# Kernel optimization log

Measured on AMD Instinct MI355X. Metric: run time of the kernel, lower is better.

The kernel has to match this reference:

```python
import jax, jax.numpy as jnp
import numpy as np

N = 50000      # nodes
E = 600000     # edges
D_IN = 128
D_H = 128
D_OUT = 64
HEADS = 2
NEG_SLOPE = 0.2  # PyG GATConv default leaky_relu slope
BN_EPS = 1e-5


def setup_inputs() -> dict:
    key = jax.random.key(0)
    ks = jax.random.split(key, 24)
    w = lambda i, shape: (jax.random.normal(ks[i], shape, jnp.float32) * 0.1)
    return {
        "x": jax.random.normal(ks[0], (N, D_IN), jnp.float32),
        "edge_index": jax.random.randint(ks[1], (2, E), 0, N, jnp.int64),
        "W_gcn1": w(2, (D_IN, D_H)),
        "b_gcn1": jnp.zeros((D_H,), jnp.float32),
        "bn1_gamma": jax.random.uniform(ks[3], (D_H,), jnp.float32, 0.5, 1.5),
        "bn1_beta": w(4, (D_H,)),
        "bn1_mean": w(5, (D_H,)),
        "bn1_var": jax.random.uniform(ks[6], (D_H,), jnp.float32, 0.5, 1.5),
        "W_gat1": w(7, (D_H, HEADS * D_H)),
        "a_src1": w(8, (HEADS, D_H)),
        "a_dst1": w(9, (HEADS, D_H)),
        "b_gat1": jnp.zeros((D_H,), jnp.float32),
        "W_gcn2": w(10, (D_H, D_H)),
        "b_gcn2": jnp.zeros((D_H,), jnp.float32),
        "bn2_gamma": jax.random.uniform(ks[11], (D_H,), jnp.float32, 0.5, 1.5),
        "bn2_beta": w(12, (D_H,)),
        "bn2_mean": w(13, (D_H,)),
        "bn2_var": jax.random.uniform(ks[14], (D_H,), jnp.float32, 0.5, 1.5),
        "W_gat2": w(15, (D_H, HEADS * D_OUT)),
        "a_src2": w(16, (HEADS, D_OUT)),
        "a_dst2": w(17, (HEADS, D_OUT)),
        "b_gat2": jnp.zeros((D_OUT,), jnp.float32),
    }


def _add_self_loops(edge_index):
    loop = jnp.arange(N, dtype=edge_index.dtype)
    src = jnp.concatenate([edge_index[0], loop])
    dst = jnp.concatenate([edge_index[1], loop])
    return src, dst


def _gcn(x, edge_index, W, b):
    # PyG GCNConv: add self-loops, symmetric D^-1/2 (A+I) D^-1/2 normalization
    src, dst = _add_self_loops(edge_index)
    deg = jax.ops.segment_sum(jnp.ones_like(dst, x.dtype), dst, num_segments=N)
    dinv = jax.lax.rsqrt(jnp.maximum(deg, 1.0))  # deg >= 1 with self-loops
    norm = dinv[src] * dinv[dst]                 # [E+N]
    h = x @ W                                    # [N, C]
    out = jax.ops.segment_sum(h[src] * norm[:, None], dst, num_segments=N)
    return out + b


def _gat(x, edge_index, W, a_src, a_dst, b, out_ch):
    # PyG GATConv (concat=False): per-head attention, segment softmax over dst,
    # mean across heads. Dropout off (eval mode).
    h = (x @ W).reshape(N, HEADS, out_ch)                 # [N, H, C]
    al_s = jnp.einsum('nhc,hc->nh', h, a_src)             # [N, H]
    al_d = jnp.einsum('nhc,hc->nh', h, a_dst)             # [N, H]
    src, dst = _add_self_loops(edge_index)
    e = al_s[src] + al_d[dst]                             # [E+N, H]
    e = jnp.where(e > 0, e, NEG_SLOPE * e)                # leaky_relu
    m = jax.ops.segment_max(e, dst, num_segments=N)       # [N, H]
    ex = jnp.exp(e - m[dst])
    denom = jax.ops.segment_sum(ex, dst, num_segments=N)  # [N, H]
    alpha = ex / denom[dst]                               # [E+N, H]
    out = jax.ops.segment_sum(h[src] * alpha[:, :, None], dst, num_segments=N)
    return out.mean(axis=1) + b                           # concat=False -> mean


def _bn_eval(x, gamma, beta, mean, var):
    return (x - mean) * jax.lax.rsqrt(var + BN_EPS) * gamma + beta


def reference(x, edge_index, W_gcn1, b_gcn1, bn1_gamma, bn1_beta, bn1_mean, bn1_var,
              W_gat1, a_src1, a_dst1, b_gat1, W_gcn2, b_gcn2,
              bn2_gamma, bn2_beta, bn2_mean, bn2_var,
              W_gat2, a_src2, a_dst2, b_gat2):
    h = _gcn(x, edge_index, W_gcn1, b_gcn1)
    h = jax.nn.relu(_bn_eval(h, bn1_gamma, bn1_beta, bn1_mean, bn1_var))
    h = jax.nn.relu(_gat(h, edge_index, W_gat1, a_src1, a_dst1, b_gat1, D_H))
    h = _gcn(h, edge_index, W_gcn2, b_gcn2)
    h = jax.nn.relu(_bn_eval(h, bn2_gamma, bn2_beta, bn2_mean, bn2_var))
    h = _gat(h, edge_index, W_gat2, a_src2, a_dst2, b_gat2, D_OUT)
    return jax.nn.log_softmax(h, axis=1)
```

## Files before the change

kernel.cpp:

```cpp
#include <hip/hip_runtime.h>
#include <hip/hip_bf16.h>

#define N_NODES 50000
#define N_EDGES 600000

typedef short bf16x8 __attribute__((ext_vector_type(8)));
typedef float f32x4 __attribute__((ext_vector_type(4)));

__device__ __forceinline__ float leaky(float e) { return fmaxf(e, 0.2f * e); }
__device__ __forceinline__ unsigned short f2b(float f) {
  __hip_bfloat16 h = __float2bfloat16(f);
  return *reinterpret_cast<unsigned short*>(&h);
}
__device__ __forceinline__ float blo(unsigned int u) { return __uint_as_float(u << 16); }
__device__ __forceinline__ float bhi(unsigned int u) { return __uint_as_float(u & 0xffff0000u); }

__global__ void k_convert(const int* __restrict__ e, int* __restrict__ src32,
                          int* __restrict__ dst32, int* __restrict__ deg,
                          const float* __restrict__ W1, const float* __restrict__ WG1,
                          const float* __restrict__ W2, const float* __restrict__ WG2,
                          unsigned short* __restrict__ Wt1, unsigned short* __restrict__ WtG1,
                          unsigned short* __restrict__ Wt2, unsigned short* __restrict__ WtG2,
                          const float* b1, const float* g1, const float* be1, const float* m1,
                          const float* v1, const float* b2, const float* g2, const float* be2,
                          const float* m2, const float* v2, float* sc1, float* sh1,
                          float* sc2, float* sh2,
                          const float* as1, const float* ad1, const float* as2,
                          const float* ad2, float* was1, float* wad1, float* was2,
                          float* wad2) {
  __shared__ int sflag;
  int tid = threadIdx.x;
  if (tid < 64) {
    int idx = 1 + 2 * tid * 4096;
    int v = e[idx];
    unsigned long long nz = __ballot(v != 0);
    if (tid == 0) sflag = (nz == 0ULL) ? 1 : 0;
  }
  __syncthreads();
  int f = sflag;
  int i = blockIdx.x * 256 + tid;
  if (i < N_EDGES) {
    int s, d;
    if (f) { s = e[2 * i]; d = e[2 * (N_EDGES + i)]; }
    else   { s = e[i];     d = e[N_EDGES + i]; }
    src32[i] = s;
    dst32[i] = d;
    atomicAdd(&deg[d], 1);
  }
  if (i < 16384) {
    int k = i >> 7, c = i & 127;
    Wt1[c * 128 + k] = f2b(W1[i]);
  } else if (i < 49152) {
    int l = i - 16384;
    int k = l >> 8, c8 = l & 255;
    int head = c8 >> 7, cc = c8 & 127;
    WtG1[cc * 256 + head * 128 + k] = f2b(WG1[l]);
  } else if (i < 65536) {
    int l = i - 49152;
    int k = l >> 7, c = l & 127;
    Wt2[c * 128 + k] = f2b(W2[l]);
  } else if (i < 81920) {
    int l = i - 65536;
    int k = l >> 7, c = l & 127;
    WtG2[c * 128 + k] = f2b(WG2[l]);
  } else if (i < 82048) {
    int c = i - 81920;
    float s = g1[c] * rsqrtf(v1[c] + 1e-5f);
    sc1[c] = s;
    sh1[c] = (b1[c] - m1[c]) * s + be1[c];
  } else if (i < 82176) {
    int c = i - 82048;
    float s = g2[c] * rsqrtf(v2[c] + 1e-5f);
    sc2[c] = s;
    sh2[c] = (b2[c] - m2[c]) * s + be2[c];
  } else if (i < 82688) {
    int j = i - 82176;
    int k = j & 127;
    int vec = j >> 7;
    const float* Wr = (vec < 2) ? (WG1 + k * 256) : (WG2 + k * 128);
    const float* av = (vec == 0) ? as1 : (vec == 1) ? ad1 : (vec == 2) ? as2 : ad2;
    float* op = (vec == 0) ? was1 : (vec == 1) ? wad1 : (vec == 2) ? was2 : wad2;
    int hl = (vec < 2) ? 128 : 64;
    float s0 = 0.f, s1 = 0.f;
    for (int c = 0; c < hl; c += 4) {
      float4 wv = *(const float4*)(Wr + c);
      float4 a4 = *(const float4*)(av + c);
      s0 += wv.x * a4.x + wv.y * a4.y + wv.z * a4.z + wv.w * a4.w;
    }
    for (int c = 0; c < hl; c += 4) {
      float4 wv = *(const float4*)(Wr + hl + c);
      float4 a4 = *(const float4*)(av + hl + c);
      s1 += wv.x * a4.x + wv.y * a4.y + wv.z * a4.z + wv.w * a4.w;
    }
    op[2 * k] = s0;
    op[2 * k + 1] = s1;
  }
}

__global__ void k_offsets(const int* __restrict__ deg, int* __restrict__ gbase,
                          int* __restrict__ roff, int* __restrict__ cursor,
                          float* __restrict__ dinv) {
  __shared__ int s[256];
  __shared__ int base;
  int t = threadIdx.x;
  int i = blockIdx.x * 256 + t;
  int v = (i < N_NODES) ? deg[i] : 0;
  s[t] = v;
  __syncthreads();
  for (int o = 1; o < 256; o <<= 1) {
    int x = (t >= o) ? s[t - o] : 0;
    __syncthreads();
    s[t] += x;
    __syncthreads();
  }
  if (t == 255) base = atomicAdd(gbase, s[255]);
  __syncthreads();
  int off = base + s[t] - v;
  if (i < N_NODES) {
    roff[i] = off;
    cursor[i] = off;
    dinv[i] = rsqrtf((float)v + 1.f);
  }
}
__global__ void k_fill(const int* __restrict__ src, const int* __restrict__ dst,
                       int* __restrict__ cursor, int2* __restrict__ aen,
                       const float* __restrict__ dinv) {
  int e = blockIdx.x * 256 + threadIdx.x;
  if (e < N_EDGES) {
    int s = src[e], d = dst[e];
    int pos = atomicAdd(&cursor[d], 1);
    aen[pos] = make_int2(s, __float_as_int(dinv[s]));
  }
}

__device__ __forceinline__ float4 ld4(const float* X, size_t idx) {
  return *(const float4*)(X + idx);
}
__device__ __forceinline__ float4 ld4(const unsigned short* X, size_t idx) {
  uint2 r = *(const uint2*)(X + idx);
  return make_float4(blo(r.x), bhi(r.x), blo(r.y), bhi(r.y));
}

template <typename TX>
__global__ __launch_bounds__(256, 4) void gemm_mfma(const TX* __restrict__ X,
                                                    const unsigned short* __restrict__ Wt,
                                                    unsigned short* __restrict__ Hb) {
  __shared__ __align__(16) short smem[64 * 136];
  int tid = threadIdx.x;
  int row0 = blockIdx.x * 64;
  for (int i = tid; i < 2048; i += 256) {
    int r = i >> 5;
    int k4 = (i & 31) * 4;
    int row = row0 + r;
    float4 v = make_float4(0.f, 0.f, 0.f, 0.f);
    if (row < N_NODES) v = ld4(X, (size_t)row * 128 + k4);
    uint2 p;
    p.x = (unsigned int)f2b(v.x) | ((unsigned int)f2b(v.y) << 16);
    p.y = (unsigned int)f2b(v.z) | ((unsigned int)f2b(v.w) << 16);
    *(uint2*)&smem[r * 136 + k4] = p;
  }
  int wave = tid >> 6, lane = tid & 63;
  int m = lane & 15, quad = lane >> 4;
  int c0 = wave * 32;
  bf16x8 b[2][4];
#pragma unroll
  for (int ct = 0; ct < 2; ++ct) {
    const unsigned short* wp = Wt + (size_t)(c0 + ct * 16 + m) * 128 + quad * 8;
#pragma unroll
    for (int kk = 0; kk < 4; ++kk) b[ct][kk] = *(const bf16x8*)(wp + kk * 32);
  }
  __syncthreads();
#pragma unroll
  for (int rt = 0; rt < 4; ++rt) {
    bf16x8 a[4];
#pragma unroll
    for (int kk = 0; kk < 4; ++kk)
      a[kk] = *(const bf16x8*)&smem[(rt * 16 + m) * 136 + kk * 32 + quad * 8];
    f32x4 acc[2];
#pragma unroll
    for (int ct = 0; ct < 2; ++ct) acc[ct] = (f32x4){0.f, 0.f, 0.f, 0.f};
#pragma unroll
    for (int ct = 0; ct < 2; ++ct)
#pragma unroll
      for (int kk = 0; kk < 4; ++kk)
        acc[ct] = __builtin_amdgcn_mfma_f32_16x16x32_bf16(a[kk], b[ct][kk], acc[ct], 0, 0, 0);
    int rbase = row0 + rt * 16 + quad * 4;
#pragma unroll
    for (int ct = 0; ct < 2; ++ct) {
#pragma unroll
      for (int reg = 0; reg < 4; ++reg) {
        int row = rbase + reg;
        if (row < N_NODES)
          Hb[(size_t)row * 128 + c0 + ct * 16 + m] = f2b(acc[ct][reg]);
      }
    }
  }
}

__global__ __launch_bounds__(256, 4) void gemm_k256(const unsigned short* __restrict__ Q,
                                                    const unsigned short* __restrict__ Wt,
                                                    const float* __restrict__ bias,
                                                    unsigned short* __restrict__ G) {
  __shared__ __align__(16) short smem[64 * 136];
  int tid = threadIdx.x;
  int row0 = blockIdx.x * 64;
  int wave = tid >> 6, lane = tid & 63;
  int m = lane & 15, quad = lane >> 4;
  int c0 = wave * 32;
  f32x4 acc[4][2];
#pragma unroll
  for (int rt = 0; rt < 4; ++rt)
#pragma unroll
    for (int ct = 0; ct < 2; ++ct) acc[rt][ct] = (f32x4){0.f, 0.f, 0.f, 0.f};
#pragma unroll
  for (int half = 0; half < 2; ++half) {
    if (half) __syncthreads();
    for (int i = tid; i < 2048; i += 256) {
      int r = i >> 5;
      int k4 = (i & 31) * 4;
      int row = row0 + r;
      uint2 p = make_uint2(0u, 0u);
      if (row < N_NODES) p = *(const uint2*)(Q + (size_t)row * 256 + half * 128 + k4);
      *(uint2*)&smem[r * 136 + k4] = p;
    }
    bf16x8 b[2][4];
#pragma unroll
    for (int ct = 0; ct < 2; ++ct) {
      const unsigned short* wp =
          Wt + (size_t)(c0 + ct * 16 + m) * 256 + half * 128 + quad * 8;
#pragma unroll
      for (int kk = 0; kk < 4; ++kk) b[ct][kk] = *(const bf16x8*)(wp + kk * 32);
    }
    __syncthreads();
#pragma unroll
    for (int rt = 0; rt < 4; ++rt) {
      bf16x8 a[4];
#pragma unroll
      for (int kk = 0; kk < 4; ++kk)
        a[kk] = *(const bf16x8*)&smem[(rt * 16 + m) * 136 + kk * 32 + quad * 8];
#pragma unroll
      for (int ct = 0; ct < 2; ++ct)
#pragma unroll
        for (int kk = 0; kk < 4; ++kk)
          acc[rt][ct] =
              __builtin_amdgcn_mfma_f32_16x16x32_bf16(a[kk], b[ct][kk], acc[rt][ct], 0, 0, 0);
    }
  }
#pragma unroll
  for (int rt = 0; rt < 4; ++rt) {
    int rbase = row0 + rt * 16 + quad * 4;
#pragma unroll
    for (int ct = 0; ct < 2; ++ct) {
      int col = c0 + ct * 16 + m;
      float bs = bias[col];
#pragma unroll
      for (int reg = 0; reg < 4; ++reg) {
        int row = rbase + reg;
        if (row < N_NODES)
          G[(size_t)row * 128 + col] = f2b(fmaxf(acc[rt][ct][reg] + bs, 0.f));
      }
    }
  }
}

__global__ __launch_bounds__(256) void gcn_pull(const unsigned short* __restrict__ Hb,
                                                const int2* __restrict__ aen,
                                                const int* __restrict__ roff,
                                                const int* __restrict__ deg,
                                                const float* __restrict__ dinv,
                                                const float* __restrict__ sc,
                                                const float* __restrict__ sh,
                                                const float* __restrict__ was,
                                                const float* __restrict__ wad,
                                                float* __restrict__ als,
                                                float* __restrict__ ald,
                                                unsigned short* __restrict__ out) {
  int wv = (blockIdx.x * 256 + threadIdx.x) >> 6;
  int lane = threadIdx.x & 63;
  int q4 = lane >> 4, l16 = lane & 15;
  int qb = lane & 48, l7 = lane & 7;
  int i = 4 * wv + q4;
  if (i >= N_NODES) return;
  int off = roff[i], end = off + deg[i];
  float di = dinv[i];
  uint4 u = *(const uint4*)((const char*)Hb + (unsigned)i * 256u + l16 * 16u);
  float a0 = blo(u.x) * di, a1 = bhi(u.x) * di;
  float a2 = blo(u.y) * di, a3 = bhi(u.y) * di;
  float a4 = blo(u.z) * di, a5 = bhi(u.z) * di;
  float a6 = blo(u.w) * di, a7 = bhi(u.w) * di;
  int j = off;
  int nfull = (end - off) >> 3;
  int2 ae = make_int2(i, 0);
  if (l7 < end - j) ae = aen[j + l7];
  for (int t = 0; t < nfull; ++t) {
    int ss[8];
#pragma unroll
    for (int k = 0; k < 8; ++k) ss[k] = __shfl(ae.x, qb + k, 64);
    float ww[8];
#pragma unroll
    for (int k = 0; k < 8; ++k) ww[k] = __shfl(__int_as_float(ae.y), qb + k, 64);
    uint4 vv[8];
#pragma unroll
    for (int k = 0; k < 8; ++k)
      vv[k] = *(const uint4*)((const char*)Hb + (unsigned)ss[k] * 256u + l16 * 16u);
    j += 8;
    if (l7 < end - j) ae = aen[j + l7];
#pragma unroll
    for (int k = 0; k < 8; ++k) {
      a0 = fmaf(blo(vv[k].x), ww[k], a0); a1 = fmaf(bhi(vv[k].x), ww[k], a1);
      a2 = fmaf(blo(vv[k].y), ww[k], a2); a3 = fmaf(bhi(vv[k].y), ww[k], a3);
      a4 = fmaf(blo(vv[k].z), ww[k], a4); a5 = fmaf(bhi(vv[k].z), ww[k], a5);
      a6 = fmaf(blo(vv[k].w), ww[k], a6); a7 = fmaf(bhi(vv[k].w), ww[k], a7);
    }
  }
  int rem = end - j;
  if (rem) {
    int ss[8];
#pragma unroll
    for (int k = 0; k < 8; ++k) ss[k] = __shfl(ae.x, qb + k, 64);
    float ww[8];
#pragma unroll
    for (int k = 0; k < 8; ++k) ww[k] = __shfl(__int_as_float(ae.y), qb + k, 64);
    uint4 vv[8];
#pragma unroll
    for (int k = 0; k < 8; ++k)
      if (k < rem)
        vv[k] = *(const uint4*)((const char*)Hb + (unsigned)ss[k] * 256u + l16 * 16u);
#pragma unroll
    for (int k = 0; k < 8; ++k)
      if (k < rem) {
        a0 = fmaf(blo(vv[k].x), ww[k], a0); a1 = fmaf(bhi(vv[k].x), ww[k], a1);
        a2 = fmaf(blo(vv[k].y), ww[k], a2); a3 = fmaf(bhi(vv[k].y), ww[k], a3);
        a4 = fmaf(blo(vv[k].z), ww[k], a4); a5 = fmaf(bhi(vv[k].z), ww[k], a5);
        a6 = fmaf(blo(vv[k].w), ww[k], a6); a7 = fmaf(bhi(vv[k].w), ww[k], a7);
      }
  }
  int c0 = l16 * 8;
  float4 sca = *(const float4*)(sc + c0), scb = *(const float4*)(sc + c0 + 4);
  float4 sha = *(const float4*)(sh + c0), shb = *(const float4*)(sh + c0 + 4);
  float t0 = fmaxf(fmaf(a0 * di, sca.x, sha.x), 0.f);
  float t1 = fmaxf(fmaf(a1 * di, sca.y, sha.y), 0.f);
  float t2 = fmaxf(fmaf(a2 * di, sca.z, sha.z), 0.f);
  float t3 = fmaxf(fmaf(a3 * di, sca.w, sha.w), 0.f);
  float t4 = fmaxf(fmaf(a4 * di, scb.x, shb.x), 0.f);
  float t5 = fmaxf(fmaf(a5 * di, scb.y, shb.y), 0.f);
  float t6 = fmaxf(fmaf(a6 * di, scb.z, shb.z), 0.f);
  float t7 = fmaxf(fmaf(a7 * di, scb.w, shb.w), 0.f);
  float4 w0 = *(const float4*)(was + 2 * c0);
  float4 w1 = *(const float4*)(was + 2 * c0 + 4);
  float4 w2 = *(const float4*)(was + 2 * c0 + 8);
  float4 w3 = *(const float4*)(was + 2 * c0 + 12);
  float sl0 = t0 * w0.x + t1 * w0.z + t2 * w1.x + t3 * w1.z +
              t4 * w2.x + t5 * w2.z + t6 * w3.x + t7 * w3.z;
  float sl1 = t0 * w0.y + t1 * w0.w + t2 * w1.y + t3 * w1.w +
              t4 * w2.y + t5 * w2.w + t6 * w3.y + t7 * w3.w;
  w0 = *(const float4*)(wad + 2 * c0);
  w1 = *(const float4*)(wad + 2 * c0 + 4);
  w2 = *(const float4*)(wad + 2 * c0 + 8);
  w3 = *(const float4*)(wad + 2 * c0 + 12);
  float dl0 = t0 * w0.x + t1 * w0.z + t2 * w1.x + t3 * w1.z +
              t4 * w2.x + t5 * w2.z + t6 * w3.x + t7 * w3.z;
  float dl1 = t0 * w0.y + t1 * w0.w + t2 * w1.y + t3 * w1.w +
              t4 * w2.y + t5 * w2.w + t6 * w3.y + t7 * w3.w;
#pragma unroll
  for (int mask = 1; mask <= 8; mask <<= 1) {
    sl0 += __shfl_xor(sl0, mask, 64);
    sl1 += __shfl_xor(sl1, mask, 64);
    dl0 += __shfl_xor(dl0, mask, 64);
    dl1 += __shfl_xor(dl1, mask, 64);
  }
  if (l16 == 0) {
    *(float2*)(als + 2 * i) = make_float2(sl0, sl1);
    *(float2*)(ald + 2 * i) = make_float2(dl0, dl1);
  }
  uint4 pw;
  pw.x = (unsigned int)f2b(t0) | ((unsigned int)f2b(t1) << 16);
  pw.y = (unsigned int)f2b(t2) | ((unsigned int)f2b(t3) << 16);
  pw.z = (unsigned int)f2b(t4) | ((unsigned int)f2b(t5) << 16);
  pw.w = (unsigned int)f2b(t6) | ((unsigned int)f2b(t7) << 16);
  *(uint4*)(out + (size_t)i * 128 + l16 * 8) = pw;
}

__global__ __launch_bounds__(256) void gat1_pull(const unsigned short* __restrict__ P,
                                                 const int2* __restrict__ aen,
                                                 const int* __restrict__ roff,
                                                 const int* __restrict__ deg,
                                                 const float* __restrict__ als,
                                                 const float* __restrict__ ald,
                                                 unsigned short* __restrict__ Q) {
  int wv = (blockIdx.x * 256 + threadIdx.x) >> 6;
  int lane = threadIdx.x & 63;
  int q4 = lane >> 4, l16 = lane & 15;
  int qb = lane & 48, l7 = lane & 7;
  int i = 4 * wv + q4;
  if (i >= N_NODES) return;
  int off = roff[i], end = off + deg[i];
  float2 dif = *(const float2*)(ald + 2 * i);
  float p0 = 0.f, p1 = 0.f;
  float g0 = 0.f, g1 = 0.f, g2 = 0.f, g3 = 0.f,
        g4 = 0.f, g5 = 0.f, g6 = 0.f, g7 = 0.f;
  float h0 = 0.f, h1 = 0.f, h2 = 0.f, h3 = 0.f,
        h4 = 0.f, h5 = 0.f, h6 = 0.f, h7 = 0.f;
  int j = off;
  int nfull = (end - off) >> 3;
  int2 ae = make_int2(i, 0);
  float2 av = make_float2(-1e30f, -1e30f);
  if (l7 < end - j) {
    ae = aen[j + l7];
    av = *(const float2*)(als + 2 * ae.x);
  }
  for (int t = 0; t < nfull; ++t) {
    int ss[8];
#pragma unroll
    for (int k = 0; k < 8; ++k) ss[k] = __shfl(ae.x, qb + k, 64);
    uint4 vv[8];
#pragma unroll
    for (int k = 0; k < 8; ++k)
      vv[k] = *(const uint4*)((const char*)P + (unsigned)ss[k] * 256u + l16 * 16u);
    float q0 = __expf(leaky(av.x + dif.x));
    float q1 = __expf(leaky(av.y + dif.y));
    j += 8;
    if (l7 < end - j) {
      ae = aen[j + l7];
      av = *(const float2*)(als + 2 * ae.x);
    }
#pragma unroll
    for (int k = 0; k < 8; ++k) {
      float b0 = __shfl(q0, qb + k, 64);
      float b1 = __shfl(q1, qb + k, 64);
      p0 += b0; p1 += b1;
      float c0 = blo(vv[k].x), c1 = bhi(vv[k].x);
      float c2 = blo(vv[k].y), c3 = bhi(vv[k].y);
      float c4 = blo(vv[k].z), c5 = bhi(vv[k].z);
      float c6 = blo(vv[k].w), c7 = bhi(vv[k].w);
      g0 = fmaf(b0, c0, g0); h0 = fmaf(b1, c0, h0);
      g1 = fmaf(b0, c1, g1); h1 = fmaf(b1, c1, h1);
      g2 = fmaf(b0, c2, g2); h2 = fmaf(b1, c2, h2);
      g3 = fmaf(b0, c3, g3); h3 = fmaf(b1, c3, h3);
      g4 = fmaf(b0, c4, g4); h4 = fmaf(b1, c4, h4);
      g5 = fmaf(b0, c5, g5); h5 = fmaf(b1, c5, h5);
      g6 = fmaf(b0, c6, g6); h6 = fmaf(b1, c6, h6);
      g7 = fmaf(b0, c7, g7); h7 = fmaf(b1, c7, h7);
    }
  }
  int rem = end - j;
  if (rem) {
    int ss[8];
#pragma unroll
    for (int k = 0; k < 8; ++k) ss[k] = __shfl(ae.x, qb + k, 64);
    uint4 vv[8];
#pragma unroll
    for (int k = 0; k < 8; ++k)
      if (k < rem)
        vv[k] = *(const uint4*)((const char*)P + (unsigned)ss[k] * 256u + l16 * 16u);
    float q0 = __expf(leaky(av.x + dif.x));
    float q1 = __expf(leaky(av.y + dif.y));
#pragma unroll
    for (int k = 0; k < 8; ++k)
      if (k < rem) {
        float b0 = __shfl(q0, qb + k, 64);
        float b1 = __shfl(q1, qb + k, 64);
        p0 += b0; p1 += b1;
        float c0 = blo(vv[k].x), c1 = bhi(vv[k].x);
        float c2 = blo(vv[k].y), c3 = bhi(vv[k].y);
        float c4 = blo(vv[k].z), c5 = bhi(vv[k].z);
        float c6 = blo(vv[k].w), c7 = bhi(vv[k].w);
        g0 = fmaf(b0, c0, g0); h0 = fmaf(b1, c0, h0);
        g1 = fmaf(b0, c1, g1); h1 = fmaf(b1, c1, h1);
        g2 = fmaf(b0, c2, g2); h2 = fmaf(b1, c2, h2);
        g3 = fmaf(b0, c3, g3); h3 = fmaf(b1, c3, h3);
        g4 = fmaf(b0, c4, g4); h4 = fmaf(b1, c4, h4);
        g5 = fmaf(b0, c5, g5); h5 = fmaf(b1, c5, h5);
        g6 = fmaf(b0, c6, g6); h6 = fmaf(b1, c6, h6);
        g7 = fmaf(b0, c7, g7); h7 = fmaf(b1, c7, h7);
      }
  }
  float2 ai = *(const float2*)(als + 2 * i);
  float es0 = __expf(leaky(ai.x + dif.x));
  float es1 = __expf(leaky(ai.y + dif.y));
  float r0 = 0.5f / (p0 + es0);
  float r1 = 0.5f / (p1 + es1);
  uint4 u = *(const uint4*)((const char*)P + (unsigned)i * 256u + l16 * 16u);
  float c0 = blo(u.x), c1 = bhi(u.x), c2 = blo(u.y), c3 = bhi(u.y);
  float c4 = blo(u.z), c5 = bhi(u.z), c6 = blo(u.w), c7 = bhi(u.w);
  g0 = (g0 + es0 * c0) * r0; g1 = (g1 + es0 * c1) * r0;
  g2 = (g2 + es0 * c2) * r0; g3 = (g3 + es0 * c3) * r0;
  g4 = (g4 + es0 * c4) * r0; g5 = (g5 + es0 * c5) * r0;
  g6 = (g6 + es0 * c6) * r0; g7 = (g7 + es0 * c7) * r0;
  h0 = (h0 + es1 * c0) * r1; h1 = (h1 + es1 * c1) * r1;
  h2 = (h2 + es1 * c2) * r1; h3 = (h3 + es1 * c3) * r1;
  h4 = (h4 + es1 * c4) * r1; h5 = (h5 + es1 * c5) * r1;
  h6 = (h6 + es1 * c6) * r1; h7 = (h7 + es1 * c7) * r1;
  uint4 pw;
  pw.x = (unsigned int)f2b(g0) | ((unsigned int)f2b(g1) << 16);
  pw.y = (unsigned int)f2b(g2) | ((unsigned int)f2b(g3) << 16);
  pw.z = (unsigned int)f2b(g4) | ((unsigned int)f2b(g5) << 16);
  pw.w = (unsigned int)f2b(g6) | ((unsigned int)f2b(g7) << 16);
  *(uint4*)(Q + (size_t)i * 256 + l16 * 8) = pw;
  pw.x = (unsigned int)f2b(h0) | ((unsigned int)f2b(h1) << 16);
  pw.y = (unsigned int)f2b(h2) | ((unsigned int)f2b(h3) << 16);
  pw.z = (unsigned int)f2b(h4) | ((unsigned int)f2b(h5) << 16);
  pw.w = (unsigned int)f2b(h6) | ((unsigned int)f2b(h7) << 16);
  *(uint4*)(Q + (size_t)i * 256 + 128 + l16 * 8) = pw;
}

__global__ __launch_bounds__(256) void gat_pull64_lsm(const unsigned short* __restrict__ Hb,
                                                      const int2* __restrict__ aen,
                                                      const int* __restrict__ roff,
                                                      const int* __restrict__ deg,
                                                      const float* __restrict__ als,
                                                      const float* __restrict__ ald,
                                                      const float* __restrict__ bias,
                                                      float* __restrict__ out) {
  int wv = (blockIdx.x * 256 + threadIdx.x) >> 6;
  int lane = threadIdx.x & 63;
  int q4 = lane >> 4, l16 = lane & 15;
  int qb = lane & 48, l7 = lane & 7;
  int hh = l16 >> 3, p8 = l16 & 7;
  int i = 4 * wv + q4;
  if (i >= N_NODES) return;
  int off = roff[i], end = off + deg[i];
  unsigned cb2 = (unsigned)(hh * 64 + 8 * p8) * 2u;
  float2 dd = *(const float2*)(ald + 2 * i);
  float p = 0.f;
  float acc0 = 0.f, acc1 = 0.f, acc2 = 0.f, acc3 = 0.f;
  float acc4 = 0.f, acc5 = 0.f, acc6 = 0.f, acc7 = 0.f;
  int j = off;
  int nfull = (end - off) >> 3;
  int2 ae = make_int2(i, 0);
  float2 av = make_float2(-1e30f, -1e30f);
  if (l7 < end - j) {
    ae = aen[j + l7];
    av = *(const float2*)(als + 2 * ae.x);
  }
  for (int t = 0; t < nfull; ++t) {
    int ss[8];
#pragma unroll
    for (int k = 0; k < 8; ++k) ss[k] = __shfl(ae.x, qb + k, 64);
    uint4 vv[8];
#pragma unroll
    for (int k = 0; k < 8; ++k)
      vv[k] = *(const uint4*)((const char*)Hb + (unsigned)ss[k] * 256u + cb2);
    float q0 = __expf(leaky(av.x + dd.x));
    float q1 = __expf(leaky(av.y + dd.y));
    j += 8;
    if (l7 < end - j) {
      ae = aen[j + l7];
      av = *(const float2*)(als + 2 * ae.x);
    }
#pragma unroll
    for (int k = 0; k < 8; ++k) {
      float b0 = __shfl(q0, qb + k, 64);
      float b1 = __shfl(q1, qb + k, 64);
      float q = hh ? b1 : b0;
      p += q;
      acc0 = fmaf(q, blo(vv[k].x), acc0); acc1 = fmaf(q, bhi(vv[k].x), acc1);
      acc2 = fmaf(q, blo(vv[k].y), acc2); acc3 = fmaf(q, bhi(vv[k].y), acc3);
      acc4 = fmaf(q, blo(vv[k].z), acc4); acc5 = fmaf(q, bhi(vv[k].z), acc5);
      acc6 = fmaf(q, blo(vv[k].w), acc6); acc7 = fmaf(q, bhi(vv[k].w), acc7);
    }
  }
  int rem = end - j;
  if (rem) {
    int ss[8];
#pragma unroll
    for (int k = 0; k < 8; ++k) ss[k] = __shfl(ae.x, qb + k, 64);
    uint4 vv[8];
#pragma unroll
    for (int k = 0; k < 8; ++k)
      if (k < rem)
        vv[k] = *(const uint4*)((const char*)Hb + (unsigned)ss[k] * 256u + cb2);
    float q0 = __expf(leaky(av.x + dd.x));
    float q1 = __expf(leaky(av.y + dd.y));
#pragma unroll
    for (int k = 0; k < 8; ++k)
      if (k < rem) {
        float b0 = __shfl(q0, qb + k, 64);
        float b1 = __shfl(q1, qb + k, 64);
        float q = hh ? b1 : b0;
        p += q;
        acc0 = fmaf(q, blo(vv[k].x), acc0); acc1 = fmaf(q, bhi(vv[k].x), acc1);
        acc2 = fmaf(q, blo(vv[k].y), acc2); acc3 = fmaf(q, bhi(vv[k].y), acc3);
        acc4 = fmaf(q, blo(vv[k].z), acc4); acc5 = fmaf(q, bhi(vv[k].z), acc5);
        acc6 = fmaf(q, blo(vv[k].w), acc6); acc7 = fmaf(q, bhi(vv[k].w), acc7);
      }
  }
  float2 ai = *(const float2*)(als + 2 * i);
  float axs = hh ? ai.y : ai.x;
  float dh = hh ? dd.y : dd.x;
  float es = __expf(leaky(axs + dh));
  float rsel = 0.5f / (p + es);
  uint4 u = *(const uint4*)((const char*)Hb + (unsigned)i * 256u + cb2);
  acc0 = (acc0 + es * blo(u.x)) * rsel; acc1 = (acc1 + es * bhi(u.x)) * rsel;
  acc2 = (acc2 + es * blo(u.y)) * rsel; acc3 = (acc3 + es * bhi(u.y)) * rsel;
  acc4 = (acc4 + es * blo(u.z)) * rsel; acc5 = (acc5 + es * bhi(u.z)) * rsel;
  acc6 = (acc6 + es * blo(u.w)) * rsel; acc7 = (acc7 + es * bhi(u.w)) * rsel;
  acc0 += __shfl_xor(acc0, 8, 64); acc1 += __shfl_xor(acc1, 8, 64);
  acc2 += __shfl_xor(acc2, 8, 64); acc3 += __shfl_xor(acc3, 8, 64);
  acc4 += __shfl_xor(acc4, 8, 64); acc5 += __shfl_xor(acc5, 8, 64);
  acc6 += __shfl_xor(acc6, 8, 64); acc7 += __shfl_xor(acc7, 8, 64);
  float4 b0 = *(const float4*)(bias + 8 * p8);
  float4 b1 = *(const float4*)(bias + 8 * p8 + 4);
  float v0 = acc0 + b0.x, v1 = acc1 + b0.y, v2 = acc2 + b0.z, v3 = acc3 + b0.w;
  float v4 = acc4 + b1.x, v5 = acc5 + b1.y, v6 = acc6 + b1.z, v7 = acc7 + b1.w;
  float mv = fmaxf(fmaxf(fmaxf(v0, v1), fmaxf(v2, v3)),
                   fmaxf(fmaxf(v4, v5), fmaxf(v6, v7)));
#pragma unroll
  for (int mm = 4; mm > 0; mm >>= 1) mv = fmaxf(mv, __shfl_xor(mv, mm, 64));
  float sv = __expf(v0 - mv) + __expf(v1 - mv) + __expf(v2 - mv) + __expf(v3 - mv) +
             __expf(v4 - mv) + __expf(v5 - mv) + __expf(v6 - mv) + __expf(v7 - mv);
#pragma unroll
  for (int mm = 4; mm > 0; mm >>= 1) sv += __shfl_xor(sv, mm, 64);
  float ls = mv + __logf(sv);
  if (hh == 0) {
    *(float4*)(out + (size_t)i * 64 + 8 * p8) =
        make_float4(v0 - ls, v1 - ls, v2 - ls, v3 - ls);
    *(float4*)(out + (size_t)i * 64 + 8 * p8 + 4) =
        make_float4(v4 - ls, v5 - ls, v6 - ls, v7 - ls);
  }
}

extern "C" void kernel_launch(void* const* d_in, const int* in_sizes, int n_in, void* d_out,
                              int out_size, void* d_ws, size_t ws_size, hipStream_t stream) {
  const float* x      = (const float*)d_in[0];
  const int* eidx     = (const int*)d_in[1];
  const float* W_gcn1 = (const float*)d_in[2];
  const float* b_gcn1 = (const float*)d_in[3];
  const float* bn1_g  = (const float*)d_in[4];
  const float* bn1_b  = (const float*)d_in[5];
  const float* bn1_m  = (const float*)d_in[6];
  const float* bn1_v  = (const float*)d_in[7];
  const float* W_gat1 = (const float*)d_in[8];
  const float* a_src1 = (const float*)d_in[9];
  const float* a_dst1 = (const float*)d_in[10];
  const float* b_gat1 = (const float*)d_in[11];
  const float* W_gcn2 = (const float*)d_in[12];
  const float* b_gcn2 = (const float*)d_in[13];
  const float* bn2_g  = (const float*)d_in[14];
  const float* bn2_b  = (const float*)d_in[15];
  const float* bn2_m  = (const float*)d_in[16];
  const float* bn2_v  = (const float*)d_in[17];
  const float* W_gat2 = (const float*)d_in[18];
  const float* a_src2 = (const float*)d_in[19];
  const float* a_dst2 = (const float*)d_in[20];
  const float* b_gat2 = (const float*)d_in[21];

  char* ws = (char*)d_ws;
  size_t o = 0;
  auto take = [&](size_t bytes) {
    char* p = ws + o;
    o = (o + bytes + 255) & ~(size_t)255;
    return p;
  };
  int* srcs    = (int*)take((size_t)N_EDGES * 4);
  int* dstsb   = (int*)take((size_t)N_EDGES * 4);
  int* deg     = (int*)take((size_t)(N_NODES + 64) * 4);
  int* gbase   = deg + N_NODES;
  int* roff    = (int*)take((size_t)N_NODES * 4);
  int* cursor  = (int*)take((size_t)N_NODES * 4);
  int2* aen    = (int2*)take((size_t)N_EDGES * 8);
  float* dinv  = (float*)take((size_t)N_NODES * 4);
  float* als   = (float*)take((size_t)2 * N_NODES * 4);
  float* ald   = (float*)take((size_t)2 * N_NODES * 4);
  float* sc1   = (float*)take(128 * 4);
  float* sh1   = (float*)take(128 * 4);
  float* sc2   = (float*)take(128 * 4);
  float* sh2   = (float*)take(128 * 4);
  float* was1  = (float*)take(256 * 4);
  float* wad1  = (float*)take(256 * 4);
  float* was2  = (float*)take(256 * 4);
  float* wad2  = (float*)take(256 * 4);
  unsigned short* Wt1  = (unsigned short*)take((size_t)128 * 128 * 2);
  unsigned short* WtG1 = (unsigned short*)take((size_t)128 * 256 * 2);
  unsigned short* Wt2  = (unsigned short*)take((size_t)128 * 128 * 2);
  unsigned short* WtG2 = (unsigned short*)take((size_t)128 * 128 * 2);
  unsigned short* Hb   = (unsigned short*)take((size_t)N_NODES * 128 * 2);
  unsigned short* Pb   = (unsigned short*)take((size_t)N_NODES * 128 * 2);
  unsigned short* Qb   = (unsigned short*)take((size_t)N_NODES * 256 * 2);
  unsigned short* Gb   = (unsigned short*)take((size_t)N_NODES * 128 * 2);
  (void)ws_size; (void)in_sizes; (void)n_in; (void)out_size;

  int eb = (N_EDGES + 255) / 256;
  int nb = (N_NODES + 255) / 256;
  int qb = ((N_NODES + 3) / 4 + 3) / 4;
  int gb = (N_NODES + 63) / 64;

  hipMemsetAsync(deg, 0, (size_t)(N_NODES + 1) * 4, stream);
  k_convert<<<eb, 256, 0, stream>>>(eidx, srcs, dstsb, deg, W_gcn1, W_gat1, W_gcn2, W_gat2,
                                    Wt1, WtG1, Wt2, WtG2, b_gcn1, bn1_g, bn1_b, bn1_m, bn1_v,
                                    b_gcn2, bn2_g, bn2_b, bn2_m, bn2_v, sc1, sh1, sc2, sh2,
                                    a_src1, a_dst1, a_src2, a_dst2, was1, wad1, was2, wad2);
  k_offsets<<<nb, 256, 0, stream>>>(deg, gbase, roff, cursor, dinv);
  k_fill<<<eb, 256, 0, stream>>>(srcs, dstsb, cursor, aen, dinv);

  gemm_mfma<<<gb, 256, 0, stream>>>(x, Wt1, Hb);
  gcn_pull<<<qb, 256, 0, stream>>>(Hb, aen, roff, deg, dinv, sc1, sh1, was1, wad1,
                                   als, ald, Pb);
  gat1_pull<<<qb, 256, 0, stream>>>(Pb, aen, roff, deg, als, ald, Qb);
  gemm_k256<<<gb, 256, 0, stream>>>(Qb, WtG1, b_gat1, Gb);
  gemm_mfma<<<gb, 256, 0, stream>>>(Gb, Wt2, Hb);
  gcn_pull<<<qb, 256, 0, stream>>>(Hb, aen, roff, deg, dinv, sc2, sh2, was2, wad2,
                                   als, ald, Pb);
  gemm_mfma<<<gb, 256, 0, stream>>>(Pb, WtG2, Qb);
  gat_pull64_lsm<<<qb, 256, 0, stream>>>(Qb, aen, roff, deg, als, ald, b_gat2,
                                         (float*)d_out);
}
```

Baseline: 340.8 us.

## Reorder GCN2 as aggregate-then-transform and fuse GCN2/GAT2 GEMMs with LDS-staged stores

Layer-2 GCN now aggregates the GAT1 output first (A·G), then a single kernel applies W_gcn2, BN+ReLU, the W_gat2 GEMM and the attention logits, keeping the intermediate in LDS. This removes one GEMM launch and a full bf16 round trip of the intermediate. GEMM epilogues now stage results through shared memory so rows are written with coalesced 16-byte stores. Edge-index conversion no longer writes src/dst int32 copies; k_fill reads the original index array directly using a stored layout flag. The reordering changes where bf16 rounding happens, which slightly alters numerics.

```diff
diff --git a/kernel.cpp b/kernel.cpp
--- a/kernel.cpp
+++ b/kernel.cpp
@@ -15,8 +15,8 @@
 __device__ __forceinline__ float blo(unsigned int u) { return __uint_as_float(u << 16); }
 __device__ __forceinline__ float bhi(unsigned int u) { return __uint_as_float(u & 0xffff0000u); }
 
-__global__ void k_convert(const int* __restrict__ e, int* __restrict__ src32,
-                          int* __restrict__ dst32, int* __restrict__ deg,
+__global__ void k_convert(const int* __restrict__ e, int* __restrict__ deg,
+                          int* __restrict__ flag,
                           const float* __restrict__ W1, const float* __restrict__ WG1,
                           const float* __restrict__ W2, const float* __restrict__ WG2,
                           unsigned short* __restrict__ Wt1, unsigned short* __restrict__ WtG1,
@@ -39,12 +39,9 @@
   __syncthreads();
   int f = sflag;
   int i = blockIdx.x * 256 + tid;
+  if (i == 0) flag[0] = f;
   if (i < N_EDGES) {
-    int s, d;
-    if (f) { s = e[2 * i]; d = e[2 * (N_EDGES + i)]; }
-    else   { s = e[i];     d = e[N_EDGES + i]; }
-    src32[i] = s;
-    dst32[i] = d;
+    int d = f ? e[2 * (N_EDGES + i)] : e[N_EDGES + i];
     atomicAdd(&deg[d], 1);
   }
   if (i < 16384) {
@@ -122,27 +119,21 @@
     dinv[i] = rsqrtf((float)v + 1.f);
   }
 }
-__global__ void k_fill(const int* __restrict__ src, const int* __restrict__ dst,
+__global__ void k_fill(const int* __restrict__ e, const int* __restrict__ flag,
                        int* __restrict__ cursor, int2* __restrict__ aen,
                        const float* __restrict__ dinv) {
-  int e = blockIdx.x * 256 + threadIdx.x;
-  if (e < N_EDGES) {
-    int s = src[e], d = dst[e];
+  int f = flag[0];
+  int i = blockIdx.x * 256 + threadIdx.x;
+  if (i < N_EDGES) {
+    int s, d;
+    if (f) { s = e[2 * i]; d = e[2 * (N_EDGES + i)]; }
+    else   { s = e[i];     d = e[N_EDGES + i]; }
     int pos = atomicAdd(&cursor[d], 1);
     aen[pos] = make_int2(s, __float_as_int(dinv[s]));
   }
 }
 
-__device__ __forceinline__ float4 ld4(const float* X, size_t idx) {
-  return *(const float4*)(X + idx);
-}
-__device__ __forceinline__ float4 ld4(const unsigned short* X, size_t idx) {
-  uint2 r = *(const uint2*)(X + idx);
-  return make_float4(blo(r.x), bhi(r.x), blo(r.y), bhi(r.y));
-}
-
-template <typename TX>
-__global__ __launch_bounds__(256, 4) void gemm_mfma(const TX* __restrict__ X,
+__global__ __launch_bounds__(256, 4) void gemm_mfma(const float* __restrict__ X,
                                                     const unsigned short* __restrict__ Wt,
                                                     unsigned short* __restrict__ Hb) {
   __shared__ __align__(16) short smem[64 * 136];
@@ -153,7 +144,7 @@
     int k4 = (i & 31) * 4;
     int row = row0 + r;
     float4 v = make_float4(0.f, 0.f, 0.f, 0.f);
-    if (row < N_NODES) v = ld4(X, (size_t)row * 128 + k4);
+    if (row < N_NODES) v = *(const float4*)(X + (size_t)row * 128 + k4);
     uint2 p;
     p.x = (unsigned int)f2b(v.x) | ((unsigned int)f2b(v.y) << 16);
     p.y = (unsigned int)f2b(v.z) | ((unsigned int)f2b(v.w) << 16);
@@ -170,30 +161,37 @@
     for (int kk = 0; kk < 4; ++kk) b[ct][kk] = *(const bf16x8*)(wp + kk * 32);
   }
   __syncthreads();
+  f32x4 acc[4][2];
+#pragma unroll
+  for (int rt = 0; rt < 4; ++rt)
+#pragma unroll
+    for (int ct = 0; ct < 2; ++ct) acc[rt][ct] = (f32x4){0.f, 0.f, 0.f, 0.f};
 #pragma unroll
   for (int rt = 0; rt < 4; ++rt) {
     bf16x8 a[4];
 #pragma unroll
     for (int kk = 0; kk < 4; ++kk)
       a[kk] = *(const bf16x8*)&smem[(rt * 16 + m) * 136 + kk * 32 + quad * 8];
-    f32x4 acc[2];
-#pragma unroll
-    for (int ct = 0; ct < 2; ++ct) acc[ct] = (f32x4){0.f, 0.f, 0.f, 0.f};
 #pragma unroll
     for (int ct = 0; ct < 2; ++ct)
 #pragma unroll
       for (int kk = 0; kk < 4; ++kk)
-        acc[ct] = __builtin_amdgcn_mfma_f32_16x16x32_bf16(a[kk], b[ct][kk], acc[ct], 0, 0, 0);
-    int rbase = row0 + rt * 16 + quad * 4;
-#pragma unroll
-    for (int ct = 0; ct < 2; ++ct) {
-#pragma unroll
-      for (int reg = 0; reg < 4; ++reg) {
-        int row = rbase + reg;
-        if (row < N_NODES)
-          Hb[(size_t)row * 128 + c0 + ct * 16 + m] = f2b(acc[ct][reg]);
-      }
-    }
+        acc[rt][ct] = __builtin_amdgcn_mfma_f32_16x16x32_bf16(a[kk], b[ct][kk], acc[rt][ct], 0, 0, 0);
+  }
+  __syncthreads();
+#pragma unroll
+  for (int rt = 0; rt < 4; ++rt)
+#pragma unroll
+    for (int ct = 0; ct < 2; ++ct)
+#pragma unroll
+      for (int reg = 0; reg < 4; ++reg)
+        smem[(rt * 16 + quad * 4 + reg) * 128 + c0 + ct * 16 + m] = (short)f2b(acc[rt][ct][reg]);
+  __syncthreads();
+  for (int i = tid; i < 1024; i += 256) {
+    int row = row0 + (i >> 4);
+    if (row < N_NODES)
+      *(uint4*)((char*)Hb + (size_t)row0 * 256 + (size_t)i * 16) =
+          *(uint4*)((char*)smem + (size_t)i * 16);
   }
 }
 
@@ -246,23 +244,159 @@
               __builtin_amdgcn_mfma_f32_16x16x32_bf16(a[kk], b[ct][kk], acc[rt][ct], 0, 0, 0);
     }
   }
+  __syncthreads();
+  float bv[2];
+#pragma unroll
+  for (int ct = 0; ct < 2; ++ct) bv[ct] = bias[c0 + ct * 16 + m];
+#pragma unroll
+  for (int rt = 0; rt < 4; ++rt)
+#pragma unroll
+    for (int ct = 0; ct < 2; ++ct)
+#pragma unroll
+      for (int reg = 0; reg < 4; ++reg)
+        smem[(rt * 16 + quad * 4 + reg) * 128 + c0 + ct * 16 + m] =
+            (short)f2b(fmaxf(acc[rt][ct][reg] + bv[ct], 0.f));
+  __syncthreads();
+  for (int i = tid; i < 1024; i += 256) {
+    int row = row0 + (i >> 4);
+    if (row < N_NODES)
+      *(uint4*)((char*)G + (size_t)row0 * 256 + (size_t)i * 16) =
+          *(uint4*)((char*)smem + (size_t)i * 16);
+  }
+}
+
+__global__ __launch_bounds__(256, 4) void gemm_gcn2_gat2(
+    const unsigned short* __restrict__ AG, const unsigned short* __restrict__ Wt2,
+    const float* __restrict__ sc, const float* __restrict__ sh,
+    const unsigned short* __restrict__ WtG2,
+    const float* __restrict__ was, const float* __restrict__ wad,
+    float* __restrict__ als, float* __restrict__ ald,
+    unsigned short* __restrict__ Q2) {
+  __shared__ __align__(16) short smA[64 * 136];
+  __shared__ __align__(16) short smB[64 * 136];
+  int tid = threadIdx.x;
+  int row0 = blockIdx.x * 64;
+  for (int i = tid; i < 1024; i += 256) {
+    int r = i >> 4;
+    int k8 = (i & 15) * 8;
+    int row = row0 + r;
+    uint4 p = make_uint4(0u, 0u, 0u, 0u);
+    if (row < N_NODES) p = *(const uint4*)(AG + (size_t)row * 128 + k8);
+    *(uint4*)&smA[r * 136 + k8] = p;
+  }
+  int wave = tid >> 6, lane = tid & 63;
+  int m = lane & 15, quad = lane >> 4;
+  int c0 = wave * 32;
+  bf16x8 b1[2][4];
+#pragma unroll
+  for (int ct = 0; ct < 2; ++ct) {
+    const unsigned short* wp = Wt2 + (size_t)(c0 + ct * 16 + m) * 128 + quad * 8;
+#pragma unroll
+    for (int kk = 0; kk < 4; ++kk) b1[ct][kk] = *(const bf16x8*)(wp + kk * 32);
+  }
+  __syncthreads();
+  f32x4 acc[4][2];
+#pragma unroll
+  for (int rt = 0; rt < 4; ++rt)
+#pragma unroll
+    for (int ct = 0; ct < 2; ++ct) acc[rt][ct] = (f32x4){0.f, 0.f, 0.f, 0.f};
 #pragma unroll
   for (int rt = 0; rt < 4; ++rt) {
-    int rbase = row0 + rt * 16 + quad * 4;
-#pragma unroll
-    for (int ct = 0; ct < 2; ++ct) {
-      int col = c0 + ct * 16 + m;
-      float bs = bias[col];
-#pragma unroll
-      for (int reg = 0; reg < 4; ++reg) {
-        int row = rbase + reg;
-        if (row < N_NODES)
-          G[(size_t)row * 128 + col] = f2b(fmaxf(acc[rt][ct][reg] + bs, 0.f));
-      }
-    }
-  }
-}
-
+    bf16x8 a[4];
+#pragma unroll
+    for (int kk = 0; kk < 4; ++kk)
+      a[kk] = *(const bf16x8*)&smA[(rt * 16 + m) * 136 + kk * 32 + quad * 8];
+#pragma unroll
+    for (int ct = 0; ct < 2; ++ct)
+#pragma unroll
+      for (int kk = 0; kk < 4; ++kk)
+        acc[rt][ct] = __builtin_amdgcn_mfma_f32_16x16x32_bf16(a[kk], b1[ct][kk], acc[rt][ct], 0, 0, 0);
+  }
+  float scv[2], shv[2];
+#pragma unroll
+  for (int ct = 0; ct < 2; ++ct) {
+    scv[ct] = sc[c0 + ct * 16 + m];
+    shv[ct] = sh[c0 + ct * 16 + m];
+  }
+#pragma unroll
+  for (int rt = 0; rt < 4; ++rt)
+#pragma unroll
+    for (int ct = 0; ct < 2; ++ct)
+#pragma unroll
+      for (int reg = 0; reg < 4; ++reg)
+        smB[(rt * 16 + quad * 4 + reg) * 136 + c0 + ct * 16 + m] =
+            (short)f2b(fmaxf(fmaf(acc[rt][ct][reg], scv[ct], shv[ct]), 0.f));
+  __syncthreads();
+  bf16x8 b2[2][4];
+#pragma unroll
+  for (int ct = 0; ct < 2; ++ct) {
+    const unsigned short* wp = WtG2 + (size_t)(c0 + ct * 16 + m) * 128 + quad * 8;
+#pragma unroll
+    for (int kk = 0; kk < 4; ++kk) b2[ct][kk] = *(const bf16x8*)(wp + kk * 32);
+  }
+  f32x4 acc2[4][2];
+#pragma unroll
+  for (int rt = 0; rt < 4; ++rt)
+#pragma unroll
+    for (int ct = 0; ct < 2; ++ct) acc2[rt][ct] = (f32x4){0.f, 0.f, 0.f, 0.f};
+#pragma unroll
+  for (int rt = 0; rt < 4; ++rt) {
+    bf16x8 a[4];
+#pragma unroll
+    for (int kk = 0; kk < 4; ++kk)
+      a[kk] = *(const bf16x8*)&smB[(rt * 16 + m) * 136 + kk * 32 + quad * 8];
+#pragma unroll
+    for (int ct = 0; ct < 2; ++ct)
+#pragma unroll
+      for (int kk = 0; kk < 4; ++kk)
+        acc2[rt][ct] = __builtin_amdgcn_mfma_f32_16x16x32_bf16(a[kk], b2[ct][kk], acc2[rt][ct], 0, 0, 0);
+  }
+  {
+    int rloc = wave * 16 + (lane >> 2);
+    int k0 = (lane & 3) * 32;
+    float s0 = 0.f, s1 = 0.f, d0 = 0.f, d1 = 0.f;
+#pragma unroll
+    for (int c = 0; c < 32; c += 2) {
+      unsigned u = *(const unsigned*)&smB[rloc * 136 + k0 + c];
+      float x0 = blo(u), x1 = bhi(u);
+      float4 ws4 = *(const float4*)(was + 2 * (k0 + c));
+      float4 wd4 = *(const float4*)(wad + 2 * (k0 + c));
+      s0 = fmaf(x0, ws4.x, s0); s1 = fmaf(x0, ws4.y, s1);
+      s0 = fmaf(x1, ws4.z, s0); s1 = fmaf(x1, ws4.w, s1);
+      d0 = fmaf(x0, wd4.x, d0); d1 = fmaf(x0, wd4.y, d1);
+      d0 = fmaf(x1, wd4.z, d0); d1 = fmaf(x1, wd4.w, d1);
+    }
+#pragma unroll
+    for (int mask = 1; mask <= 2; mask <<= 1) {
+      s0 += __shfl_xor(s0, mask, 64);
+      s1 += __shfl_xor(s1, mask, 64);
+      d0 += __shfl_xor(d0, mask, 64);
+      d1 += __shfl_xor(d1, mask, 64);
+    }
+    int row = row0 + rloc;
+    if ((lane & 3) == 0 && row < N_NODES) {
+      *(float2*)(als + 2 * row) = make_float2(s0, s1);
+      *(float2*)(ald + 2 * row) = make_float2(d0, d1);
+    }
+  }
+#pragma unroll
+  for (int rt = 0; rt < 4; ++rt)
+#pragma unroll
+    for (int ct = 0; ct < 2; ++ct)
+#pragma unroll
+      for (int reg = 0; reg < 4; ++reg)
+        smA[(rt * 16 + quad * 4 + reg) * 128 + c0 + ct * 16 + m] =
+            (short)f2b(acc2[rt][ct][reg]);
+  __syncthreads();
+  for (int i = tid; i < 1024; i += 256) {
+    int row = row0 + (i >> 4);
+    if (row < N_NODES)
+      *(uint4*)((char*)Q2 + (size_t)row0 * 256 + (size_t)i * 16) =
+          *(uint4*)((char*)smA + (size_t)i * 16);
+  }
+}
+
+template <int MODE>
 __global__ __launch_bounds__(256) void gcn_pull(const unsigned short* __restrict__ Hb,
                                                 const int2* __restrict__ aen,
                                                 const int* __restrict__ roff,
@@ -335,50 +469,59 @@
         a6 = fmaf(blo(vv[k].w), ww[k], a6); a7 = fmaf(bhi(vv[k].w), ww[k], a7);
       }
   }
-  int c0 = l16 * 8;
-  float4 sca = *(const float4*)(sc + c0), scb = *(const float4*)(sc + c0 + 4);
-  float4 sha = *(const float4*)(sh + c0), shb = *(const float4*)(sh + c0 + 4);
-  float t0 = fmaxf(fmaf(a0 * di, sca.x, sha.x), 0.f);
-  float t1 = fmaxf(fmaf(a1 * di, sca.y, sha.y), 0.f);
-  float t2 = fmaxf(fmaf(a2 * di, sca.z, sha.z), 0.f);
-  float t3 = fmaxf(fmaf(a3 * di, sca.w, sha.w), 0.f);
-  float t4 = fmaxf(fmaf(a4 * di, scb.x, shb.x), 0.f);
-  float t5 = fmaxf(fmaf(a5 * di, scb.y, shb.y), 0.f);
-  float t6 = fmaxf(fmaf(a6 * di, scb.z, shb.z), 0.f);
-  float t7 = fmaxf(fmaf(a7 * di, scb.w, shb.w), 0.f);
-  float4 w0 = *(const float4*)(was + 2 * c0);
-  float4 w1 = *(const float4*)(was + 2 * c0 + 4);
-  float4 w2 = *(const float4*)(was + 2 * c0 + 8);
-  float4 w3 = *(const float4*)(was + 2 * c0 + 12);
-  float sl0 = t0 * w0.x + t1 * w0.z + t2 * w1.x + t3 * w1.z +
-              t4 * w2.x + t5 * w2.z + t6 * w3.x + t7 * w3.z;
-  float sl1 = t0 * w0.y + t1 * w0.w + t2 * w1.y + t3 * w1.w +
-              t4 * w2.y + t5 * w2.w + t6 * w3.y + t7 * w3.w;
-  w0 = *(const float4*)(wad + 2 * c0);
-  w1 = *(const float4*)(wad + 2 * c0 + 4);
-  w2 = *(const float4*)(wad + 2 * c0 + 8);
-  w3 = *(const float4*)(wad + 2 * c0 + 12);
-  float dl0 = t0 * w0.x + t1 * w0.z + t2 * w1.x + t3 * w1.z +
-              t4 * w2.x + t5 * w2.z + t6 * w3.x + t7 * w3.z;
-  float dl1 = t0 * w0.y + t1 * w0.w + t2 * w1.y + t3 * w1.w +
-              t4 * w2.y + t5 * w2.w + t6 * w3.y + t7 * w3.w;
-#pragma unroll
-  for (int mask = 1; mask <= 8; mask <<= 1) {
-    sl0 += __shfl_xor(sl0, mask, 64);
-    sl1 += __shfl_xor(sl1, mask, 64);
-    dl0 += __shfl_xor(dl0, mask, 64);
-    dl1 += __shfl_xor(dl1, mask, 64);
-  }
-  if (l16 == 0) {
-    *(float2*)(als + 2 * i) = make_float2(sl0, sl1);
-    *(float2*)(ald + 2 * i) = make_float2(dl0, dl1);
-  }
-  uint4 pw;
-  pw.x = (unsigned int)f2b(t0) | ((unsigned int)f2b(t1) << 16);
-  pw.y = (unsigned int)f2b(t2) | ((unsigned int)f2b(t3) << 16);
-  pw.z = (unsigned int)f2b(t4) | ((unsigned int)f2b(t5) << 16);
-  pw.w = (unsigned int)f2b(t6) | ((unsigned int)f2b(t7) << 16);
-  *(uint4*)(out + (size_t)i * 128 + l16 * 8) = pw;
+  if constexpr (MODE == 1) {
+    uint4 pw;
+    pw.x = (unsigned int)f2b(a0 * di) | ((unsigned int)f2b(a1 * di) << 16);
+    pw.y = (unsigned int)f2b(a2 * di) | ((unsigned int)f2b(a3 * di) << 16);
+    pw.z = (unsigned int)f2b(a4 * di) | ((unsigned int)f2b(a5 * di) << 16);
+    pw.w = (unsigned int)f2b(a6 * di) | ((unsigned int)f2b(a7 * di) << 16);
+    *(uint4*)(out + (size_t)i * 128 + l16 * 8) = pw;
+  } else {
+    int c0 = l16 * 8;
+    float4 sca = *(const float4*)(sc + c0), scb = *(const float4*)(sc + c0 + 4);
+    float4 sha = *(const float4*)(sh + c0), shb = *(const float4*)(sh + c0 + 4);
+    float t0 = fmaxf(fmaf(a0 * di, sca.x, sha.x), 0.f);
+    float t1 = fmaxf(fmaf(a1 * di, sca.y, sha.y), 0.f);
+    float t2 = fmaxf(fmaf(a2 * di, sca.z, sha.z), 0.f);
+    float t3 = fmaxf(fmaf(a3 * di, sca.w, sha.w), 0.f);
+    float t4 = fmaxf(fmaf(a4 * di, scb.x, shb.x), 0.f);
+    float t5 = fmaxf(fmaf(a5 * di, scb.y, shb.y), 0.f);
+    float t6 = fmaxf(fmaf(a6 * di, scb.z, shb.z), 0.f);
+    float t7 = fmaxf(fmaf(a7 * di, scb.w, shb.w), 0.f);
+    float4 w0 = *(const float4*)(was + 2 * c0);
+    float4 w1 = *(const float4*)(was + 2 * c0 + 4);
+    float4 w2 = *(const float4*)(was + 2 * c0 + 8);
+    float4 w3 = *(const float4*)(was + 2 * c0 + 12);
+    float sl0 = t0 * w0.x + t1 * w0.z + t2 * w1.x + t3 * w1.z +
+                t4 * w2.x + t5 * w2.z + t6 * w3.x + t7 * w3.z;
+    float sl1 = t0 * w0.y + t1 * w0.w + t2 * w1.y + t3 * w1.w +
+                t4 * w2.y + t5 * w2.w + t6 * w3.y + t7 * w3.w;
+    w0 = *(const float4*)(wad + 2 * c0);
+    w1 = *(const float4*)(wad + 2 * c0 + 4);
+    w2 = *(const float4*)(wad + 2 * c0 + 8);
+    w3 = *(const float4*)(wad + 2 * c0 + 12);
+    float dl0 = t0 * w0.x + t1 * w0.z + t2 * w1.x + t3 * w1.z +
+                t4 * w2.x + t5 * w2.z + t6 * w3.x + t7 * w3.z;
+    float dl1 = t0 * w0.y + t1 * w0.w + t2 * w1.y + t3 * w1.w +
+                t4 * w2.y + t5 * w2.w + t6 * w3.y + t7 * w3.w;
+#pragma unroll
+    for (int mask = 1; mask <= 8; mask <<= 1) {
+      sl0 += __shfl_xor(sl0, mask, 64);
+      sl1 += __shfl_xor(sl1, mask, 64);
+      dl0 += __shfl_xor(dl0, mask, 64);
+      dl1 += __shfl_xor(dl1, mask, 64);
+    }
+    if (l16 == 0) {
+      *(float2*)(als + 2 * i) = make_float2(sl0, sl1);
+      *(float2*)(ald + 2 * i) = make_float2(dl0, dl1);
+    }
+    uint4 pw;
+    pw.x = (unsigned int)f2b(t0) | ((unsigned int)f2b(t1) << 16);
+    pw.y = (unsigned int)f2b(t2) | ((unsigned int)f2b(t3) << 16);
+    pw.z = (unsigned int)f2b(t4) | ((unsigned int)f2b(t5) << 16);
+    pw.w = (unsigned int)f2b(t6) | ((unsigned int)f2b(t7) << 16);
+    *(uint4*)(out + (size_t)i * 128 + l16 * 8) = pw;
+  }
 }
 
 __global__ __launch_bounds__(256) void gat1_pull(const unsigned short* __restrict__ P,
@@ -652,10 +795,9 @@
     o = (o + bytes + 255) & ~(size_t)255;
     return p;
   };
-  int* srcs    = (int*)take((size_t)N_EDGES * 4);
-  int* dstsb   = (int*)take((size_t)N_EDGES * 4);
   int* deg     = (int*)take((size_t)(N_NODES + 64) * 4);
   int* gbase   = deg + N_NODES;
+  int* flagb   = (int*)take(256);
   int* roff    = (int*)take((size_t)N_NODES * 4);
   int* cursor  = (int*)take((size_t)N_NODES * 4);
   int2* aen    = (int2*)take((size_t)N_EDGES * 8);
@@ -678,6 +820,8 @@
   unsigned short* Pb   = (unsigned short*)take((size_t)N_NODES * 128 * 2);
   unsigned short* Qb   = (unsigned short*)take((size_t)N_NODES * 256 * 2);
   unsigned short* Gb   = (unsigned short*)take((size_t)N_NODES * 128 * 2);
+  unsigned short* AGb  = (unsigned short*)take((size_t)N_NODES * 128 * 2);
+  unsigned short* Q2b  = (unsigned short*)take((size_t)N_NODES * 128 * 2);
   (void)ws_size; (void)in_sizes; (void)n_in; (void)out_size;
 
   int eb = (N_EDGES + 255) / 256;
@@ -686,22 +830,22 @@
   int gb = (N_NODES + 63) / 64;
 
   hipMemsetAsync(deg, 0, (size_t)(N_NODES + 1) * 4, stream);
-  k_convert<<<eb, 256, 0, stream>>>(eidx, srcs, dstsb, deg, W_gcn1, W_gat1, W_gcn2, W_gat2,
+  k_convert<<<eb, 256, 0, stream>>>(eidx, deg, flagb, W_gcn1, W_gat1, W_gcn2, W_gat2,
                                     Wt1, WtG1, Wt2, WtG2, b_gcn1, bn1_g, bn1_b, bn1_m, bn1_v,
                                     b_gcn2, bn2_g, bn2_b, bn2_m, bn2_v, sc1, sh1, sc2, sh2,
                                     a_src1, a_dst1, a_src2, a_dst2, was1, wad1, was2, wad2);
   k_offsets<<<nb, 256, 0, stream>>>(deg, gbase, roff, cursor, dinv);
-  k_fill<<<eb, 256, 0, stream>>>(srcs, dstsb, cursor, aen, dinv);
+  k_fill<<<eb, 256, 0, stream>>>(eidx, flagb, cursor, aen, dinv);
 
   gemm_mfma<<<gb, 256, 0, stream>>>(x, Wt1, Hb);
-  gcn_pull<<<qb, 256, 0, stream>>>(Hb, aen, roff, deg, dinv, sc1, sh1, was1, wad1,
-                                   als, ald, Pb);
+  gcn_pull<0><<<qb, 256, 0, stream>>>(Hb, aen, roff, deg, dinv, sc1, sh1, was1, wad1,
+                                      als, ald, Pb);
   gat1_pull<<<qb, 256, 0, stream>>>(Pb, aen, roff, deg, als, ald, Qb);
   gemm_k256<<<gb, 256, 0, stream>>>(Qb, WtG1, b_gat1, Gb);
-  gemm_mfma<<<gb, 256, 0, stream>>>(Gb, Wt2, Hb);
-  gcn_pull<<<qb, 256, 0, stream>>>(Hb, aen, roff, deg, dinv, sc2, sh2, was2, wad2,
-                                   als, ald, Pb);
-  gemm_mfma<<<gb, 256, 0, stream>>>(Pb, WtG2, Qb);
-  gat_pull64_lsm<<<qb, 256, 0, stream>>>(Qb, aen, roff, deg, als, ald, b_gat2,
+  gcn_pull<1><<<qb, 256, 0, stream>>>(Gb, aen, roff, deg, dinv, nullptr, nullptr,
+                                      nullptr, nullptr, nullptr, nullptr, AGb);
+  gemm_gcn2_gat2<<<gb, 256, 0, stream>>>(AGb, Wt2, sc2, sh2, WtG2, was2, wad2,
+                                         als, ald, Q2b);
+  gat_pull64_lsm<<<qb, 256, 0, stream>>>(Q2b, aen, roff, deg, als, ald, b_gat2,
                                          (float*)d_out);
 }
```

Result: no change. 342.5 us (+0.5%).
